# Optimization experiments

Measured on AMD Instinct MI355X. Metric: run time of the kernel, lower is better.

The kernel has to match this reference:

```python
import jax, jax.numpy as jnp
import numpy as np

N = 50000


def gcn_conv(x, W, b, src, dst, deg_inv_sqrt):
    # h = x @ W, then symmetric-normalized aggregation with self-loops
    h = x @ W  # [N, out]
    norm = deg_inv_sqrt[src] * deg_inv_sqrt[dst]  # [E]
    agg = jax.ops.segment_sum(h[src] * norm[:, None], dst, num_segments=N)
    # self-loop contribution: norm_ii = deg_inv_sqrt[i]^2
    agg = agg + h * (deg_inv_sqrt * deg_inv_sqrt)[:, None]
    return agg + b


def setup_inputs() -> dict:
    key = jax.random.key(0)
    ks = jax.random.split(key, 8)
    F_in, H, C = 128, 128, 64
    x = jax.random.normal(ks[0], (N, F_in), dtype=jnp.float32)
    edge_index = jax.random.randint(ks[1], (2, 800000), 0, N, dtype=jnp.int64)
    s = 1.0 / np.sqrt(F_in)
    W1 = jax.random.uniform(ks[2], (F_in, H), jnp.float32, -s, s)
    b1 = jnp.zeros((H,), jnp.float32)
    W2 = jax.random.uniform(ks[3], (H, H), jnp.float32, -s, s)
    b2 = jnp.zeros((H,), jnp.float32)
    W3 = jax.random.uniform(ks[4], (H, C), jnp.float32, -s, s)
    b3 = jnp.zeros((C,), jnp.float32)
    return {"x": x, "edge_index": edge_index, "W1": W1, "b1": b1,
            "W2": W2, "b2": b2, "W3": W3, "b3": b3}


def reference(x, edge_index, W1, b1, W2, b2, W3, b3):
    src, dst = edge_index[0], edge_index[1]
    # degree with self-loops (edge weight 1): deg[i] = in-degree + 1
    deg = jnp.zeros((N,), x.dtype).at[dst].add(1.0) + 1.0
    dinv = jax.lax.rsqrt(deg)
    h = gcn_conv(x, W1, b1, src, dst, dinv)
    h = jax.nn.relu(h)  # dropout p=0 / eval -> identity
    h = gcn_conv(h, W2, b2, src, dst, dinv)
    h = jax.nn.relu(h)
    h = gcn_conv(h, W3, b3, src, dst, dinv)
    return jax.nn.log_softmax(h, axis=-1)
```

## Files before the change

kernel.cpp:

```cpp
#include <hip/hip_runtime.h>
#include <math.h>

typedef short short8 __attribute__((ext_vector_type(8)));
typedef float floatx4 __attribute__((ext_vector_type(4)));

#define CHUNK_SHIFT 13
#define NCHUNK 8

__device__ __forceinline__ float4 ld4(const float* p) { return *reinterpret_cast<const float4*>(p); }
__device__ __forceinline__ void st4(float* p, float4 v) { *reinterpret_cast<float4*>(p) = v; }

__device__ __forceinline__ float bf2f(unsigned int u) { return __uint_as_float(u << 16); }
__device__ __forceinline__ unsigned int f2bf1(float f) {
    unsigned int x = __float_as_uint(f);
    return (x + 0x7fffu + ((x >> 16) & 1u)) >> 16;
}
__device__ __forceinline__ unsigned int f2bf2(float lo, float hi) {
    return f2bf1(lo) | (f2bf1(hi) << 16);
}
__device__ __forceinline__ void unpack8(uint4 v, float* f) {
    f[0] = bf2f(v.x & 0xffffu); f[1] = bf2f(v.x >> 16);
    f[2] = bf2f(v.y & 0xffffu); f[3] = bf2f(v.y >> 16);
    f[4] = bf2f(v.z & 0xffffu); f[5] = bf2f(v.z >> 16);
    f[6] = bf2f(v.w & 0xffffu); f[7] = bf2f(v.w >> 16);
}

__device__ __forceinline__ int sum8(const int* __restrict__ p) {
    uint4 a = *reinterpret_cast<const uint4*>(p);
    uint4 b = *reinterpret_cast<const uint4*>(p + 4);
    return (int)(a.x + a.y + a.z + a.w + b.x + b.y + b.z + b.w);
}

__global__ __launch_bounds__(256) void k_count_prep(const int* __restrict__ src, const int* __restrict__ dst,
                                                    int* __restrict__ deg2, int* __restrict__ rank, int E, int nbE,
                                                    const float* __restrict__ W1, const float* __restrict__ W2,
                                                    const float* __restrict__ W3, unsigned short* __restrict__ Wt1,
                                                    unsigned short* __restrict__ Wt2, unsigned short* __restrict__ Wt3) {
    if ((int)blockIdx.x < nbE) {
        int e = blockIdx.x * 256 + threadIdx.x;
        if (e < E) {
            int c = src[e] >> CHUNK_SHIFT;
            rank[e] = atomicAdd(&deg2[dst[e] * NCHUNK + c], 1);
        }
    } else {
        int t = (blockIdx.x - nbE) * 256 + threadIdx.x;
        if (t < 16384) {
            int k = t & 127, n = t >> 7;
            Wt1[n * 128 + k] = (unsigned short)f2bf1(W1[(size_t)k * 128 + n]);
        } else if (t < 32768) {
            int u = t - 16384;
            int k = u & 127, n = u >> 7;
            Wt2[n * 128 + k] = (unsigned short)f2bf1(W2[(size_t)k * 128 + n]);
        } else if (t < 40960) {
            int u = t - 32768;
            int k = u & 127, n = u >> 7;
            Wt3[n * 128 + k] = (unsigned short)f2bf1(W3[(size_t)k * 64 + n]);
        }
    }
}

__global__ __launch_bounds__(256) void k_dinv_reduce(const int* __restrict__ deg2, float* __restrict__ dinv,
                                                     int* __restrict__ bsum, int* __restrict__ hist,
                                                     int n, int nbN) {
    __shared__ int s[256];
    __shared__ int lh[64];
    int t = threadIdx.x;
    if ((int)blockIdx.x < nbN) {
        if (t < 64) lh[t] = 0;
        __syncthreads();
        int i = blockIdx.x * 256 + t;
        if (i < n) {
            int d = sum8(deg2 + (size_t)i * NCHUNK);
            dinv[i] = 1.0f / sqrtf((float)d + 1.0f);
            atomicAdd(&lh[min(d, 63)], 1);
        }
        __syncthreads();
        if (t < 64 && lh[t] != 0) atomicAdd(&hist[t], lh[t]);
        return;
    }
    int b = (int)blockIdx.x - nbN;
    int i = b * 256 + t;
    s[t] = (i < n) ? sum8(deg2 + (size_t)i * NCHUNK) : 0;
    __syncthreads();
    for (int off = 128; off > 0; off >>= 1) {
        if (t < off) s[t] += s[t + off];
        __syncthreads();
    }
    if (t == 0) bsum[b] = s[0];
}

__global__ __launch_bounds__(256) void k_scansmall_gemm1(const int* __restrict__ bsum, int* __restrict__ boff, int nb,
                                                         const int* __restrict__ hist, int* __restrict__ histcur,
                                                         const float* __restrict__ X, const unsigned short* __restrict__ Wt,
                                                         const float* __restrict__ dinv,
                                                         unsigned short* __restrict__ O, int nrows) {
    constexpr int LDR = 136;
    __shared__ __align__(16) unsigned char smem[(64 * LDR + 128 * LDR) * 2];

    const int tid = threadIdx.x;
    if (blockIdx.x == 0) {
        int* s = (int*)smem;
        int v = (tid < nb) ? bsum[tid] : 0;
        s[tid] = v;
        __syncthreads();
        for (int off = 1; off < 256; off <<= 1) {
            int x = (tid >= off) ? s[tid - off] : 0;
            __syncthreads();
            s[tid] += x;
            __syncthreads();
        }
        if (tid < nb) boff[tid] = s[tid] - v;
        return;
    }
    if (blockIdx.x == 1) {
        int* hsc = (int*)smem;
        if (tid < 64) hsc[tid] = hist[tid];
        __syncthreads();
        if (tid == 0) {
            int run = 0;
            for (int c = 0; c < 64; ++c) { int v = hsc[c]; hsc[c] = run; run += v; }
        }
        __syncthreads();
        if (tid < 64) histcur[tid] = hsc[tid];
        return;
    }

    unsigned short* sX = (unsigned short*)smem;
    unsigned short* sB = sX + 64 * LDR;
    const int row0 = ((int)blockIdx.x - 2) * 64;

#pragma unroll
    for (int i = 0; i < 4; ++i) {
        int idx = tid + i * 256;
        int r = idx >> 4, c8 = idx & 15;
        int grow = row0 + r;
        uint4 v = make_uint4(0, 0, 0, 0);
        if (grow < nrows) {
            float4 a = ld4(X + (size_t)grow * 128 + c8 * 8);
            float4 b = ld4(X + (size_t)grow * 128 + c8 * 8 + 4);
            v = make_uint4(f2bf2(a.x, a.y), f2bf2(a.z, a.w), f2bf2(b.x, b.y), f2bf2(b.z, b.w));
        }
        *reinterpret_cast<uint4*>(&sX[r * LDR + c8 * 8]) = v;
    }
#pragma unroll
    for (int i = 0; i < 8; ++i) {
        int idx = tid + i * 256;
        int nn = idx >> 4, c8 = idx & 15;
        *reinterpret_cast<uint4*>(&sB[nn * LDR + c8 * 8]) =
            *reinterpret_cast<const uint4*>(Wt + (size_t)nn * 128 + c8 * 8);
    }
    __syncthreads();

    const int lane = tid & 63;
    const int wave = tid >> 6;
    const int l15  = lane & 15;
    const int quad = lane >> 4;

    floatx4 acc[8];
#pragma unroll
    for (int j = 0; j < 8; ++j) acc[j] = (floatx4){0.f, 0.f, 0.f, 0.f};

    const unsigned short* xbase = &sX[(wave * 16 + l15) * LDR + quad * 8];
#pragma unroll
    for (int kk = 0; kk < 4; ++kk) {
        short8 xb = *reinterpret_cast<const short8*>(xbase + kk * 32);
#pragma unroll
        for (int j = 0; j < 8; ++j) {
            short8 wa = *reinterpret_cast<const short8*>(&sB[(j * 16 + l15) * LDR + quad * 8 + kk * 32]);
            acc[j] = __builtin_amdgcn_mfma_f32_16x16x32_bf16(wa, xb, acc[j], 0, 0, 0);
        }
    }

    int xrow = row0 + wave * 16 + l15;
    if (xrow < nrows) {
        float di = dinv[xrow];
#pragma unroll
        for (int j = 0; j < 8; ++j) {
            uint2 o = make_uint2(f2bf2(acc[j][0] * di, acc[j][1] * di), f2bf2(acc[j][2] * di, acc[j][3] * di));
            *reinterpret_cast<uint2*>(O + (size_t)xrow * 128 + j * 16 + quad * 4) = o;
        }
    }
}

__global__ __launch_bounds__(256) void k_scan_final(const int* __restrict__ deg2, const int* __restrict__ boff,
                                                    int* __restrict__ row_off, int* __restrict__ starts2,
                                                    int* __restrict__ histcur,
                                                    int* __restrict__ perm, int n, int nb) {
    __shared__ int s[256];
    __shared__ int lh[64];
    __shared__ int lbase[64];
    int t = threadIdx.x;
    if ((int)blockIdx.x < nb) {
        int i = blockIdx.x * 256 + t;
        uint4 d0 = make_uint4(0, 0, 0, 0), d1 = make_uint4(0, 0, 0, 0);
        int tot = 0;
        if (i < n) {
            d0 = *reinterpret_cast<const uint4*>(deg2 + (size_t)i * NCHUNK);
            d1 = *reinterpret_cast<const uint4*>(deg2 + (size_t)i * NCHUNK + 4);
            tot = (int)(d0.x + d0.y + d0.z + d0.w + d1.x + d1.y + d1.z + d1.w);
        }
        s[t] = tot;
        __syncthreads();
        for (int off = 1; off < 256; off <<= 1) {
            int x = (t >= off) ? s[t - off] : 0;
            __syncthreads();
            s[t] += x;
            __syncthreads();
        }
        int incl = s[t] + boff[blockIdx.x];
        if (i < n) {
            int r = incl - tot;
            row_off[i] = r;
            uint4 o0, o1;
            o0.x = r; r += d0.x;
            o0.y = r; r += d0.y;
            o0.z = r; r += d0.z;
            o0.w = r; r += d0.w;
            o1.x = r; r += d1.x;
            o1.y = r; r += d1.y;
            o1.z = r; r += d1.z;
            o1.w = r;
            *reinterpret_cast<uint4*>(starts2 + (size_t)i * NCHUNK) = o0;
            *reinterpret_cast<uint4*>(starts2 + (size_t)i * NCHUNK + 4) = o1;
            if (i == n - 1) row_off[n] = incl;
        }
        return;
    }
    int b = (int)blockIdx.x - nb;
    int i = b * 256 + t;
    if (t < 64) lh[t] = 0;
    __syncthreads();
    int c = 0, myr = 0;
    bool valid = (i < n);
    if (valid) {
        c = min(sum8(deg2 + (size_t)i * NCHUNK), 63);
        myr = atomicAdd(&lh[c], 1);
    }
    __syncthreads();
    if (t < 64 && lh[t] != 0) lbase[t] = atomicAdd(&histcur[t], lh[t]);
    __syncthreads();
    if (valid) perm[lbase[c] + myr] = i;
}

__global__ __launch_bounds__(256) void k_fill(const int* __restrict__ src, const int* __restrict__ dst,
                                              const int* __restrict__ rank, const int* __restrict__ starts2,
                                              int* __restrict__ csrc, int E) {
    int e = blockIdx.x * 256 + threadIdx.x;
    if (e < E) {
        int s = src[e];
        int c = s >> CHUNK_SHIFT;
        csrc[starts2[dst[e] * NCHUNK + c] + rank[e]] = s;
    }
}

template <int NC>
__global__ __launch_bounds__(256) void k_gemm_mfma(const unsigned short* __restrict__ X,
                                                   const unsigned short* __restrict__ Wt,
                                                   const float* __restrict__ dinv,
                                                   unsigned short* __restrict__ O, int nrows) {
    constexpr int LDR = 136;
    __shared__ unsigned short sX[64 * LDR];
    __shared__ unsigned short sB[NC * LDR];

    const int tid  = threadIdx.x;
    const int row0 = blockIdx.x * 64;

#pragma unroll
    for (int i = 0; i < 4; ++i) {
        int idx = tid + i * 256;
        int r = idx >> 4, c8 = idx & 15;
        int grow = row0 + r;
        uint4 v = make_uint4(0, 0, 0, 0);
        if (grow < nrows) v = *reinterpret_cast<const uint4*>(X + (size_t)grow * 128 + c8 * 8);
        *reinterpret_cast<uint4*>(&sX[r * LDR + c8 * 8]) = v;
    }
#pragma unroll
    for (int i = 0; i < NC / 16; ++i) {
        int idx = tid + i * 256;
        int n = idx >> 4, c8 = idx & 15;
        *reinterpret_cast<uint4*>(&sB[n * LDR + c8 * 8]) =
            *reinterpret_cast<const uint4*>(Wt + (size_t)n * 128 + c8 * 8);
    }
    __syncthreads();

    const int lane = tid & 63;
    const int wave = tid >> 6;
    const int l15  = lane & 15;
    const int quad = lane >> 4;

    floatx4 acc[NC / 16];
#pragma unroll
    for (int j = 0; j < NC / 16; ++j) acc[j] = (floatx4){0.f, 0.f, 0.f, 0.f};

    const unsigned short* xbase = &sX[(wave * 16 + l15) * LDR + quad * 8];
#pragma unroll
    for (int kk = 0; kk < 4; ++kk) {
        short8 xb = *reinterpret_cast<const short8*>(xbase + kk * 32);
#pragma unroll
        for (int j = 0; j < NC / 16; ++j) {
            short8 wa = *reinterpret_cast<const short8*>(&sB[(j * 16 + l15) * LDR + quad * 8 + kk * 32]);
            acc[j] = __builtin_amdgcn_mfma_f32_16x16x32_bf16(wa, xb, acc[j], 0, 0, 0);
        }
    }

    int xrow = row0 + wave * 16 + l15;
    if (xrow < nrows) {
        float di = dinv[xrow];
#pragma unroll
        for (int j = 0; j < NC / 16; ++j) {
            uint2 o = make_uint2(f2bf2(acc[j][0] * di, acc[j][1] * di), f2bf2(acc[j][2] * di, acc[j][3] * di));
            *reinterpret_cast<uint2*>(O + (size_t)xrow * NC + j * 16 + quad * 4) = o;
        }
    }
}

__global__ __launch_bounds__(256) void k_agg_relu(const unsigned short* __restrict__ H, const int* __restrict__ roff,
                                                  const int* __restrict__ csrc, const float* __restrict__ dinv,
                                                  const float* __restrict__ bias, const int* __restrict__ perm,
                                                  unsigned short* __restrict__ O, int n) {
    int t    = blockIdx.x * 256 + threadIdx.x;
    int g    = t >> 4;
    int f8   = (t & 15) * 8;
    if (g >= n) return;
    int node = perm[g];

    float a[8];
    {
        uint4 hv = *reinterpret_cast<const uint4*>(H + (size_t)node * 128 + f8);
        unpack8(hv, a);
    }

    int e  = roff[node];
    int e1 = roff[node + 1];
    for (; e + 3 < e1; e += 4) {
        int s[4];
        uint4 v[4];
#pragma unroll
        for (int u = 0; u < 4; ++u) s[u] = csrc[e + u];
#pragma unroll
        for (int u = 0; u < 4; ++u) v[u] = *reinterpret_cast<const uint4*>(H + (size_t)s[u] * 128 + f8);
#pragma unroll
        for (int u = 0; u < 4; ++u) {
            float g2[8];
            unpack8(v[u], g2);
#pragma unroll
            for (int i = 0; i < 8; ++i) a[i] += g2[i];
        }
    }
    for (; e < e1; ++e) {
        uint4 v0 = *reinterpret_cast<const uint4*>(H + (size_t)csrc[e] * 128 + f8);
        float g0[8];
        unpack8(v0, g0);
#pragma unroll
        for (int i = 0; i < 8; ++i) a[i] += g0[i];
    }

    float di = dinv[node];
    float4 b0 = ld4(bias + f8);
    float4 b1 = ld4(bias + f8 + 4);
    float bb[8] = {b0.x, b0.y, b0.z, b0.w, b1.x, b1.y, b1.z, b1.w};
#pragma unroll
    for (int i = 0; i < 8; ++i) a[i] = fmaxf(a[i] * di + bb[i], 0.0f);

    uint4 ov = make_uint4(f2bf2(a[0], a[1]), f2bf2(a[2], a[3]), f2bf2(a[4], a[5]), f2bf2(a[6], a[7]));
    *reinterpret_cast<uint4*>(O + (size_t)node * 128 + f8) = ov;
}

__global__ __launch_bounds__(256) void k_agg_softmax(const unsigned short* __restrict__ H, const int* __restrict__ roff,
                                                     const int* __restrict__ csrc, const float* __restrict__ dinv,
                                                     const float* __restrict__ bias, const int* __restrict__ perm,
                                                     float* __restrict__ O, int n) {
    int t    = blockIdx.x * 256 + threadIdx.x;
    int g    = t >> 3;
    int f8   = (t & 7) * 8;
    if (g >= n) return;
    int node = perm[g];

    float a[8];
    {
        uint4 hv = *reinterpret_cast<const uint4*>(H + (size_t)node * 64 + f8);
        unpack8(hv, a);
    }

    int e  = roff[node];
    int e1 = roff[node + 1];
    for (; e + 7 < e1; e += 8) {
        int s[8];
        uint4 v[8];
#pragma unroll
        for (int u = 0; u < 8; ++u) s[u] = csrc[e + u];
#pragma unroll
        for (int u = 0; u < 8; ++u) v[u] = *reinterpret_cast<const uint4*>(H + (size_t)s[u] * 64 + f8);
#pragma unroll
        for (int u = 0; u < 8; ++u) {
            float gg[8];
            unpack8(v[u], gg);
#pragma unroll
            for (int i = 0; i < 8; ++i) a[i] += gg[i];
        }
    }
    if (e + 3 < e1) {
        int s[4];
        uint4 v[4];
#pragma unroll
        for (int u = 0; u < 4; ++u) s[u] = csrc[e + u];
#pragma unroll
        for (int u = 0; u < 4; ++u) v[u] = *reinterpret_cast<const uint4*>(H + (size_t)s[u] * 64 + f8);
#pragma unroll
        for (int u = 0; u < 4; ++u) {
            float gg[8];
            unpack8(v[u], gg);
#pragma unroll
            for (int i = 0; i < 8; ++i) a[i] += gg[i];
        }
        e += 4;
    }
    for (; e < e1; ++e) {
        uint4 v0 = *reinterpret_cast<const uint4*>(H + (size_t)csrc[e] * 64 + f8);
        float g0[8];
        unpack8(v0, g0);
#pragma unroll
        for (int i = 0; i < 8; ++i) a[i] += g0[i];
    }

    float di = dinv[node];
    float4 b0 = ld4(bias + f8);
    float4 b1 = ld4(bias + f8 + 4);
    float bb[8] = {b0.x, b0.y, b0.z, b0.w, b1.x, b1.y, b1.z, b1.w};
    float v[8];
#pragma unroll
    for (int i = 0; i < 8; ++i) v[i] = a[i] * di + bb[i];

    float m = v[0];
#pragma unroll
    for (int i = 1; i < 8; ++i) m = fmaxf(m, v[i]);
    m = fmaxf(m, __shfl_xor(m, 1));
    m = fmaxf(m, __shfl_xor(m, 2));
    m = fmaxf(m, __shfl_xor(m, 4));

    float ssum = 0.0f;
#pragma unroll
    for (int i = 0; i < 8; ++i) ssum += expf(v[i] - m);
    ssum += __shfl_xor(ssum, 1);
    ssum += __shfl_xor(ssum, 2);
    ssum += __shfl_xor(ssum, 4);
    float ls = logf(ssum);

    float* op = O + (size_t)node * 64 + f8;
    st4(op, make_float4(v[0] - m - ls, v[1] - m - ls, v[2] - m - ls, v[3] - m - ls));
    st4(op + 4, make_float4(v[4] - m - ls, v[5] - m - ls, v[6] - m - ls, v[7] - m - ls));
}

extern "C" void kernel_launch(void* const* d_in, const int* in_sizes, int n_in,
                              void* d_out, int out_size, void* d_ws, size_t ws_size,
                              hipStream_t stream) {
    const float* x  = (const float*)d_in[0];
    const int*   ei = (const int*)d_in[1];
    const float* W1 = (const float*)d_in[2];
    const float* b1 = (const float*)d_in[3];
    const float* W2 = (const float*)d_in[4];
    const float* b2 = (const float*)d_in[5];
    const float* W3 = (const float*)d_in[6];
    const float* b3 = (const float*)d_in[7];
    float* out = (float*)d_out;

    const int N = in_sizes[0] / 128;
    const int E = in_sizes[1] / 2;
    const int* src = ei;
    const int* dst = ei + E;

    char* ws = (char*)d_ws;
    size_t off = 0;
    auto alloc = [&](size_t bytes) -> char* {
        char* p = ws + off;
        off = (off + bytes + 255) & ~(size_t)255;
        return p;
    };
    int nb  = (N + 255) / 256;
    int nbE = (E + 255) / 256;
    int blocks64 = (N + 63) / 64;

    int*   deg2    = (int*)alloc((size_t)N * NCHUNK * 4);
    int*   hist    = (int*)alloc(64 * 4);
    int*   histcur = (int*)alloc(64 * 4);
    int*   row_off = (int*)alloc(((size_t)N + 1) * 4);
    int*   starts2 = (int*)alloc((size_t)N * NCHUNK * 4);
    float* dinv    = (float*)alloc((size_t)N * 4);
    int*   bsum    = (int*)alloc((size_t)nb * 4);
    int*   boff    = (int*)alloc((size_t)nb * 4);
    int*   rank    = (int*)alloc((size_t)E * 4);
    int*   csrc    = (int*)alloc((size_t)E * 4);
    int*   perm    = (int*)alloc((size_t)N * 4);
    unsigned short* Wt1  = (unsigned short*)alloc(128 * 128 * 2);
    unsigned short* Wt2  = (unsigned short*)alloc(128 * 128 * 2);
    unsigned short* Wt3  = (unsigned short*)alloc(64 * 128 * 2);
    unsigned short* bufA = (unsigned short*)alloc((size_t)N * 128 * 2);
    unsigned short* bufB = (unsigned short*)alloc((size_t)N * 128 * 2);
    unsigned short* bufC = (unsigned short*)alloc((size_t)N * 64 * 2);
    (void)ws_size; (void)n_in; (void)out_size;

    size_t degPad = (((size_t)N * NCHUNK * 4 + 255) & ~(size_t)255);
    hipMemsetAsync(deg2, 0, degPad + 256, stream);
    k_count_prep<<<nbE + 160, 256, 0, stream>>>(src, dst, deg2, rank, E, nbE, W1, W2, W3, Wt1, Wt2, Wt3);
    k_dinv_reduce<<<nb + nb, 256, 0, stream>>>(deg2, dinv, bsum, hist, N, nb);
    k_scansmall_gemm1<<<2 + blocks64, 256, 0, stream>>>(bsum, boff, nb, hist, histcur, x, Wt1, dinv, bufA, N);
    k_scan_final<<<nb + nb, 256, 0, stream>>>(deg2, boff, row_off, starts2, histcur, perm, N, nb);
    k_fill<<<nbE, 256, 0, stream>>>(src, dst, rank, starts2, csrc, E);

    k_agg_relu<<<((size_t)N * 16 + 255) / 256, 256, 0, stream>>>(bufA, row_off, csrc, dinv, b1, perm, bufB, N);
    k_gemm_mfma<128><<<blocks64, 256, 0, stream>>>(bufB, Wt2, dinv, bufA, N);
    k_agg_relu<<<((size_t)N * 16 + 255) / 256, 256, 0, stream>>>(bufA, row_off, csrc, dinv, b2, perm, bufB, N);
    k_gemm_mfma<64><<<blocks64, 256, 0, stream>>>(bufB, Wt3, dinv, bufC, N);
    k_agg_softmax<<<((size_t)N * 8 + 255) / 256, 256, 0, stream>>>(bufC, row_off, csrc, dinv, b3, perm, out, N);
}
```

Measured before the change: 252.6 us.

## Fuse aggregation into following GEMM and drop degree-sorted node permutation

The separate aggregate+ReLU kernel and the MFMA GEMM kernel for layers 1 and 2 are merged into one k_agg_gemm kernel. Each block gathers neighbour rows for its 64 nodes, applies bias and ReLU, writes the bf16 result straight into shared memory and runs the MFMA from there, so the intermediate buffer never round-trips through global memory. The degree histogram and permutation sort (hist, histcur, perm) are removed entirely, and nodes are processed in natural order. The fused kernel uses only 782 blocks, and unbalanced degrees within a block cause warp divergence, so latency hiding in the gather may get worse.

```diff
diff --git a/kernel.cpp b/kernel.cpp
--- a/kernel.cpp
+++ b/kernel.cpp
@@ -60,22 +60,15 @@
 }
 
 __global__ __launch_bounds__(256) void k_dinv_reduce(const int* __restrict__ deg2, float* __restrict__ dinv,
-                                                     int* __restrict__ bsum, int* __restrict__ hist,
-                                                     int n, int nbN) {
+                                                     int* __restrict__ bsum, int n, int nbN) {
     __shared__ int s[256];
-    __shared__ int lh[64];
     int t = threadIdx.x;
     if ((int)blockIdx.x < nbN) {
-        if (t < 64) lh[t] = 0;
-        __syncthreads();
         int i = blockIdx.x * 256 + t;
         if (i < n) {
             int d = sum8(deg2 + (size_t)i * NCHUNK);
             dinv[i] = 1.0f / sqrtf((float)d + 1.0f);
-            atomicAdd(&lh[min(d, 63)], 1);
-        }
-        __syncthreads();
-        if (t < 64 && lh[t] != 0) atomicAdd(&hist[t], lh[t]);
+        }
         return;
     }
     int b = (int)blockIdx.x - nbN;
@@ -90,7 +83,6 @@
 }
 
 __global__ __launch_bounds__(256) void k_scansmall_gemm1(const int* __restrict__ bsum, int* __restrict__ boff, int nb,
-                                                         const int* __restrict__ hist, int* __restrict__ histcur,
                                                          const float* __restrict__ X, const unsigned short* __restrict__ Wt,
                                                          const float* __restrict__ dinv,
                                                          unsigned short* __restrict__ O, int nrows) {
@@ -112,22 +104,10 @@
         if (tid < nb) boff[tid] = s[tid] - v;
         return;
     }
-    if (blockIdx.x == 1) {
-        int* hsc = (int*)smem;
-        if (tid < 64) hsc[tid] = hist[tid];
-        __syncthreads();
-        if (tid == 0) {
-            int run = 0;
-            for (int c = 0; c < 64; ++c) { int v = hsc[c]; hsc[c] = run; run += v; }
-        }
-        __syncthreads();
-        if (tid < 64) histcur[tid] = hsc[tid];
-        return;
-    }
 
     unsigned short* sX = (unsigned short*)smem;
     unsigned short* sB = sX + 64 * LDR;
-    const int row0 = ((int)blockIdx.x - 2) * 64;
+    const int row0 = ((int)blockIdx.x - 1) * 64;
 
 #pragma unroll
     for (int i = 0; i < 4; ++i) {
@@ -184,62 +164,42 @@
 
 __global__ __launch_bounds__(256) void k_scan_final(const int* __restrict__ deg2, const int* __restrict__ boff,
                                                     int* __restrict__ row_off, int* __restrict__ starts2,
-                                                    int* __restrict__ histcur,
-                                                    int* __restrict__ perm, int n, int nb) {
+                                                    int n) {
     __shared__ int s[256];
-    __shared__ int lh[64];
-    __shared__ int lbase[64];
     int t = threadIdx.x;
-    if ((int)blockIdx.x < nb) {
-        int i = blockIdx.x * 256 + t;
-        uint4 d0 = make_uint4(0, 0, 0, 0), d1 = make_uint4(0, 0, 0, 0);
-        int tot = 0;
-        if (i < n) {
-            d0 = *reinterpret_cast<const uint4*>(deg2 + (size_t)i * NCHUNK);
-            d1 = *reinterpret_cast<const uint4*>(deg2 + (size_t)i * NCHUNK + 4);
-            tot = (int)(d0.x + d0.y + d0.z + d0.w + d1.x + d1.y + d1.z + d1.w);
-        }
-        s[t] = tot;
+    int i = blockIdx.x * 256 + t;
+    uint4 d0 = make_uint4(0, 0, 0, 0), d1 = make_uint4(0, 0, 0, 0);
+    int tot = 0;
+    if (i < n) {
+        d0 = *reinterpret_cast<const uint4*>(deg2 + (size_t)i * NCHUNK);
+        d1 = *reinterpret_cast<const uint4*>(deg2 + (size_t)i * NCHUNK + 4);
+        tot = (int)(d0.x + d0.y + d0.z + d0.w + d1.x + d1.y + d1.z + d1.w);
+    }
+    s[t] = tot;
+    __syncthreads();
+    for (int off = 1; off < 256; off <<= 1) {
+        int x = (t >= off) ? s[t - off] : 0;
         __syncthreads();
-        for (int off = 1; off < 256; off <<= 1) {
-            int x = (t >= off) ? s[t - off] : 0;
-            __syncthreads();
-            s[t] += x;
-            __syncthreads();
-        }
-        int incl = s[t] + boff[blockIdx.x];
-        if (i < n) {
-            int r = incl - tot;
-            row_off[i] = r;
-            uint4 o0, o1;
-            o0.x = r; r += d0.x;
-            o0.y = r; r += d0.y;
-            o0.z = r; r += d0.z;
-            o0.w = r; r += d0.w;
-            o1.x = r; r += d1.x;
-            o1.y = r; r += d1.y;
-            o1.z = r; r += d1.z;
-            o1.w = r;
-            *reinterpret_cast<uint4*>(starts2 + (size_t)i * NCHUNK) = o0;
-            *reinterpret_cast<uint4*>(starts2 + (size_t)i * NCHUNK + 4) = o1;
-            if (i == n - 1) row_off[n] = incl;
-        }
-        return;
-    }
-    int b = (int)blockIdx.x - nb;
-    int i = b * 256 + t;
-    if (t < 64) lh[t] = 0;
-    __syncthreads();
-    int c = 0, myr = 0;
-    bool valid = (i < n);
-    if (valid) {
-        c = min(sum8(deg2 + (size_t)i * NCHUNK), 63);
-        myr = atomicAdd(&lh[c], 1);
-    }
-    __syncthreads();
-    if (t < 64 && lh[t] != 0) lbase[t] = atomicAdd(&histcur[t], lh[t]);
-    __syncthreads();
-    if (valid) perm[lbase[c] + myr] = i;
+        s[t] += x;
+        __syncthreads();
+    }
+    int incl = s[t] + boff[blockIdx.x];
+    if (i < n) {
+        int r = incl - tot;
+        row_off[i] = r;
+        uint4 o0, o1;
+        o0.x = r; r += d0.x;
+        o0.y = r; r += d0.y;
+        o0.z = r; r += d0.z;
+        o0.w = r; r += d0.w;
+        o1.x = r; r += d1.x;
+        o1.y = r; r += d1.y;
+        o1.z = r; r += d1.z;
+        o1.w = r;
+        *reinterpret_cast<uint4*>(starts2 + (size_t)i * NCHUNK) = o0;
+        *reinterpret_cast<uint4*>(starts2 + (size_t)i * NCHUNK + 4) = o1;
+        if (i == n - 1) row_off[n] = incl;
+    }
 }
 
 __global__ __launch_bounds__(256) void k_fill(const int* __restrict__ src, const int* __restrict__ dst,
@@ -254,10 +214,13 @@
 }
 
 template <int NC>
-__global__ __launch_bounds__(256) void k_gemm_mfma(const unsigned short* __restrict__ X,
-                                                   const unsigned short* __restrict__ Wt,
-                                                   const float* __restrict__ dinv,
-                                                   unsigned short* __restrict__ O, int nrows) {
+__global__ __launch_bounds__(256) void k_agg_gemm(const unsigned short* __restrict__ H,
+                                                  const int* __restrict__ roff,
+                                                  const int* __restrict__ csrc,
+                                                  const float* __restrict__ dinv,
+                                                  const float* __restrict__ bias,
+                                                  const unsigned short* __restrict__ Wt,
+                                                  unsigned short* __restrict__ O, int n) {
     constexpr int LDR = 136;
     __shared__ unsigned short sX[64 * LDR];
     __shared__ unsigned short sB[NC * LDR];
@@ -266,20 +229,74 @@
     const int row0 = blockIdx.x * 64;
 
 #pragma unroll
-    for (int i = 0; i < 4; ++i) {
-        int idx = tid + i * 256;
-        int r = idx >> 4, c8 = idx & 15;
-        int grow = row0 + r;
-        uint4 v = make_uint4(0, 0, 0, 0);
-        if (grow < nrows) v = *reinterpret_cast<const uint4*>(X + (size_t)grow * 128 + c8 * 8);
-        *reinterpret_cast<uint4*>(&sX[r * LDR + c8 * 8]) = v;
-    }
-#pragma unroll
     for (int i = 0; i < NC / 16; ++i) {
         int idx = tid + i * 256;
-        int n = idx >> 4, c8 = idx & 15;
-        *reinterpret_cast<uint4*>(&sB[n * LDR + c8 * 8]) =
-            *reinterpret_cast<const uint4*>(Wt + (size_t)n * 128 + c8 * 8);
+        int nn = idx >> 4, c8 = idx & 15;
+        *reinterpret_cast<uint4*>(&sB[nn * LDR + c8 * 8]) =
+            *reinterpret_cast<const uint4*>(Wt + (size_t)nn * 128 + c8 * 8);
+    }
+
+    const int nl = tid >> 4;
+    const int f8 = (tid & 15) * 8;
+
+    float a[4][8];
+    int e[4], e1[4];
+#pragma unroll
+    for (int s = 0; s < 4; ++s) {
+        int node = row0 + s * 16 + nl;
+        if (node < n) {
+            uint4 hv = *reinterpret_cast<const uint4*>(H + (size_t)node * 128 + f8);
+            unpack8(hv, a[s]);
+            e[s]  = roff[node];
+            e1[s] = roff[node + 1];
+        } else {
+#pragma unroll
+            for (int i = 0; i < 8; ++i) a[s][i] = 0.0f;
+            e[s] = 0; e1[s] = 0;
+        }
+    }
+
+    int mb = 0;
+#pragma unroll
+    for (int s = 0; s < 4; ++s) mb = max(mb, (e1[s] - e[s] + 3) >> 2);
+
+    for (int b = 0; b < mb; ++b) {
+#pragma unroll
+        for (int s = 0; s < 4; ++s) {
+            if (e[s] >= e1[s]) continue;
+            int idx[4]; float mk[4];
+#pragma unroll
+            for (int u = 0; u < 4; ++u) {
+                bool ok = (e[s] + u) < e1[s];
+                idx[u] = ok ? csrc[e[s] + u] : 0;
+                mk[u]  = ok ? 1.0f : 0.0f;
+            }
+            uint4 v[4];
+#pragma unroll
+            for (int u = 0; u < 4; ++u) v[u] = *reinterpret_cast<const uint4*>(H + (size_t)idx[u] * 128 + f8);
+#pragma unroll
+            for (int u = 0; u < 4; ++u) {
+                float g[8];
+                unpack8(v[u], g);
+#pragma unroll
+                for (int i = 0; i < 8; ++i) a[s][i] = fmaf(mk[u], g[i], a[s][i]);
+            }
+            e[s] += 4;
+        }
+    }
+
+    float4 b0 = ld4(bias + f8);
+    float4 b1 = ld4(bias + f8 + 4);
+    float bb[8] = {b0.x, b0.y, b0.z, b0.w, b1.x, b1.y, b1.z, b1.w};
+#pragma unroll
+    for (int s = 0; s < 4; ++s) {
+        int node = row0 + s * 16 + nl;
+        float di = (node < n) ? dinv[node] : 0.0f;
+#pragma unroll
+        for (int i = 0; i < 8; ++i) a[s][i] = fmaxf(a[s][i] * di + bb[i], 0.0f);
+        uint4 ov = make_uint4(f2bf2(a[s][0], a[s][1]), f2bf2(a[s][2], a[s][3]),
+                              f2bf2(a[s][4], a[s][5]), f2bf2(a[s][6], a[s][7]));
+        *reinterpret_cast<uint4*>(&sX[(s * 16 + nl) * LDR + f8]) = ov;
     }
     __syncthreads();
 
@@ -304,7 +321,7 @@
     }
 
     int xrow = row0 + wave * 16 + l15;
-    if (xrow < nrows) {
+    if (xrow < n) {
         float di = dinv[xrow];
 #pragma unroll
         for (int j = 0; j < NC / 16; ++j) {
@@ -314,67 +331,13 @@
     }
 }
 
-__global__ __launch_bounds__(256) void k_agg_relu(const unsigned short* __restrict__ H, const int* __restrict__ roff,
-                                                  const int* __restrict__ csrc, const float* __restrict__ dinv,
-                                                  const float* __restrict__ bias, const int* __restrict__ perm,
-                                                  unsigned short* __restrict__ O, int n) {
-    int t    = blockIdx.x * 256 + threadIdx.x;
-    int g    = t >> 4;
-    int f8   = (t & 15) * 8;
-    if (g >= n) return;
-    int node = perm[g];
-
-    float a[8];
-    {
-        uint4 hv = *reinterpret_cast<const uint4*>(H + (size_t)node * 128 + f8);
-        unpack8(hv, a);
-    }
-
-    int e  = roff[node];
-    int e1 = roff[node + 1];
-    for (; e + 3 < e1; e += 4) {
-        int s[4];
-        uint4 v[4];
-#pragma unroll
-        for (int u = 0; u < 4; ++u) s[u] = csrc[e + u];
-#pragma unroll
-        for (int u = 0; u < 4; ++u) v[u] = *reinterpret_cast<const uint4*>(H + (size_t)s[u] * 128 + f8);
-#pragma unroll
-        for (int u = 0; u < 4; ++u) {
-            float g2[8];
-            unpack8(v[u], g2);
-#pragma unroll
-            for (int i = 0; i < 8; ++i) a[i] += g2[i];
-        }
-    }
-    for (; e < e1; ++e) {
-        uint4 v0 = *reinterpret_cast<const uint4*>(H + (size_t)csrc[e] * 128 + f8);
-        float g0[8];
-        unpack8(v0, g0);
-#pragma unroll
-        for (int i = 0; i < 8; ++i) a[i] += g0[i];
-    }
-
-    float di = dinv[node];
-    float4 b0 = ld4(bias + f8);
-    float4 b1 = ld4(bias + f8 + 4);
-    float bb[8] = {b0.x, b0.y, b0.z, b0.w, b1.x, b1.y, b1.z, b1.w};
-#pragma unroll
-    for (int i = 0; i < 8; ++i) a[i] = fmaxf(a[i] * di + bb[i], 0.0f);
-
-    uint4 ov = make_uint4(f2bf2(a[0], a[1]), f2bf2(a[2], a[3]), f2bf2(a[4], a[5]), f2bf2(a[6], a[7]));
-    *reinterpret_cast<uint4*>(O + (size_t)node * 128 + f8) = ov;
-}
-
 __global__ __launch_bounds__(256) void k_agg_softmax(const unsigned short* __restrict__ H, const int* __restrict__ roff,
                                                      const int* __restrict__ csrc, const float* __restrict__ dinv,
-                                                     const float* __restrict__ bias, const int* __restrict__ perm,
-                                                     float* __restrict__ O, int n) {
+                                                     const float* __restrict__ bias, float* __restrict__ O, int n) {
     int t    = blockIdx.x * 256 + threadIdx.x;
-    int g    = t >> 3;
+    int node = t >> 3;
     int f8   = (t & 7) * 8;
-    if (g >= n) return;
-    int node = perm[g];
+    if (node >= n) return;
 
     float a[8];
     {
@@ -481,8 +444,6 @@
     int blocks64 = (N + 63) / 64;
 
     int*   deg2    = (int*)alloc((size_t)N * NCHUNK * 4);
-    int*   hist    = (int*)alloc(64 * 4);
-    int*   histcur = (int*)alloc(64 * 4);
     int*   row_off = (int*)alloc(((size_t)N + 1) * 4);
     int*   starts2 = (int*)alloc((size_t)N * NCHUNK * 4);
     float* dinv    = (float*)alloc((size_t)N * 4);
@@ -490,7 +451,6 @@
     int*   boff    = (int*)alloc((size_t)nb * 4);
     int*   rank    = (int*)alloc((size_t)E * 4);
     int*   csrc    = (int*)alloc((size_t)E * 4);
-    int*   perm    = (int*)alloc((size_t)N * 4);
     unsigned short* Wt1  = (unsigned short*)alloc(128 * 128 * 2);
     unsigned short* Wt2  = (unsigned short*)alloc(128 * 128 * 2);
     unsigned short* Wt3  = (unsigned short*)alloc(64 * 128 * 2);
@@ -499,17 +459,14 @@
     unsigned short* bufC = (unsigned short*)alloc((size_t)N * 64 * 2);
     (void)ws_size; (void)n_in; (void)out_size;
 
-    size_t degPad = (((size_t)N * NCHUNK * 4 + 255) & ~(size_t)255);
-    hipMemsetAsync(deg2, 0, degPad + 256, stream);
+    hipMemsetAsync(deg2, 0, (size_t)N * NCHUNK * 4, stream);
     k_count_prep<<<nbE + 160, 256, 0, stream>>>(src, dst, deg2, rank, E, nbE, W1, W2, W3, Wt1, Wt2, Wt3);
-    k_dinv_reduce<<<nb + nb, 256, 0, stream>>>(deg2, dinv, bsum, hist, N, nb);
-    k_scansmall_gemm1<<<2 + blocks64, 256, 0, stream>>>(bsum, boff, nb, hist, histcur, x, Wt1, dinv, bufA, N);
-    k_scan_final<<<nb + nb, 256, 0, stream>>>(deg2, boff, row_off, starts2, histcur, perm, N, nb);
+    k_dinv_reduce<<<nb + nb, 256, 0, stream>>>(deg2, dinv, bsum, N, nb);
+    k_scansmall_gemm1<<<1 + blocks64, 256, 0, stream>>>(bsum, boff, nb, x, Wt1, dinv, bufA, N);
+    k_scan_final<<<nb, 256, 0, stream>>>(deg2, boff, row_off, starts2, N);
     k_fill<<<nbE, 256, 0, stream>>>(src, dst, rank, starts2, csrc, E);
 
-    k_agg_relu<<<((size_t)N * 16 + 255) / 256, 256, 0, stream>>>(bufA, row_off, csrc, dinv, b1, perm, bufB, N);
-    k_gemm_mfma<128><<<blocks64, 256, 0, stream>>>(bufB, Wt2, dinv, bufA, N);
-    k_agg_relu<<<((size_t)N * 16 + 255) / 256, 256, 0, stream>>>(bufA, row_off, csrc, dinv, b2, perm, bufB, N);
-    k_gemm_mfma<64><<<blocks64, 256, 0, stream>>>(bufB, Wt3, dinv, bufC, N);
-    k_agg_softmax<<<((size_t)N * 8 + 255) / 256, 256, 0, stream>>>(bufC, row_off, csrc, dinv, b3, perm, out, N);
-}
+    k_agg_gemm<128><<<blocks64, 256, 0, stream>>>(bufA, row_off, csrc, dinv, b1, Wt2, bufB, N);
+    k_agg_gemm<64><<<blocks64, 256, 0, stream>>>(bufB, row_off, csrc, dinv, b2, Wt3, bufC, N);
+    k_agg_softmax<<<((size_t)N * 8 + 255) / 256, 256, 0, stream>>>(bufC, row_off, csrc, dinv, b3, out, N);
+}
```

Result: slower. 271.8 us (+7.6%).

## Replace degree-sorted node permutation with split-edge two-group aggregation per node

Applied to the files above, without the earlier changes.

Removes the degree histogram, its scan and the permutation that ordered nodes by degree for load balance. Instead each node is processed by twice as many lanes, with the edge list split in half between two lane groups whose partial sums are combined by a cross-lane shuffle. This cuts several preprocessing steps and the indirect perm lookup, and doubles memory-level parallelism per node. In exchange, wavefronts can be imbalanced across differing degrees, and the second lane group idles during the epilogue.

```diff
diff --git a/kernel.cpp b/kernel.cpp
--- a/kernel.cpp
+++ b/kernel.cpp
@@ -60,22 +60,15 @@
 }
 
 __global__ __launch_bounds__(256) void k_dinv_reduce(const int* __restrict__ deg2, float* __restrict__ dinv,
-                                                     int* __restrict__ bsum, int* __restrict__ hist,
-                                                     int n, int nbN) {
+                                                     int* __restrict__ bsum, int n, int nbN) {
     __shared__ int s[256];
-    __shared__ int lh[64];
     int t = threadIdx.x;
     if ((int)blockIdx.x < nbN) {
-        if (t < 64) lh[t] = 0;
-        __syncthreads();
         int i = blockIdx.x * 256 + t;
         if (i < n) {
             int d = sum8(deg2 + (size_t)i * NCHUNK);
             dinv[i] = 1.0f / sqrtf((float)d + 1.0f);
-            atomicAdd(&lh[min(d, 63)], 1);
-        }
-        __syncthreads();
-        if (t < 64 && lh[t] != 0) atomicAdd(&hist[t], lh[t]);
+        }
         return;
     }
     int b = (int)blockIdx.x - nbN;
@@ -90,7 +83,6 @@
 }
 
 __global__ __launch_bounds__(256) void k_scansmall_gemm1(const int* __restrict__ bsum, int* __restrict__ boff, int nb,
-                                                         const int* __restrict__ hist, int* __restrict__ histcur,
                                                          const float* __restrict__ X, const unsigned short* __restrict__ Wt,
                                                          const float* __restrict__ dinv,
                                                          unsigned short* __restrict__ O, int nrows) {
@@ -112,22 +104,10 @@
         if (tid < nb) boff[tid] = s[tid] - v;
         return;
     }
-    if (blockIdx.x == 1) {
-        int* hsc = (int*)smem;
-        if (tid < 64) hsc[tid] = hist[tid];
-        __syncthreads();
-        if (tid == 0) {
-            int run = 0;
-            for (int c = 0; c < 64; ++c) { int v = hsc[c]; hsc[c] = run; run += v; }
-        }
-        __syncthreads();
-        if (tid < 64) histcur[tid] = hsc[tid];
-        return;
-    }
 
     unsigned short* sX = (unsigned short*)smem;
     unsigned short* sB = sX + 64 * LDR;
-    const int row0 = ((int)blockIdx.x - 2) * 64;
+    const int row0 = ((int)blockIdx.x - 1) * 64;
 
 #pragma unroll
     for (int i = 0; i < 4; ++i) {
@@ -184,62 +164,42 @@
 
 __global__ __launch_bounds__(256) void k_scan_final(const int* __restrict__ deg2, const int* __restrict__ boff,
                                                     int* __restrict__ row_off, int* __restrict__ starts2,
-                                                    int* __restrict__ histcur,
-                                                    int* __restrict__ perm, int n, int nb) {
+                                                    int n) {
     __shared__ int s[256];
-    __shared__ int lh[64];
-    __shared__ int lbase[64];
     int t = threadIdx.x;
-    if ((int)blockIdx.x < nb) {
-        int i = blockIdx.x * 256 + t;
-        uint4 d0 = make_uint4(0, 0, 0, 0), d1 = make_uint4(0, 0, 0, 0);
-        int tot = 0;
-        if (i < n) {
-            d0 = *reinterpret_cast<const uint4*>(deg2 + (size_t)i * NCHUNK);
-            d1 = *reinterpret_cast<const uint4*>(deg2 + (size_t)i * NCHUNK + 4);
-            tot = (int)(d0.x + d0.y + d0.z + d0.w + d1.x + d1.y + d1.z + d1.w);
-        }
-        s[t] = tot;
+    int i = blockIdx.x * 256 + t;
+    uint4 d0 = make_uint4(0, 0, 0, 0), d1 = make_uint4(0, 0, 0, 0);
+    int tot = 0;
+    if (i < n) {
+        d0 = *reinterpret_cast<const uint4*>(deg2 + (size_t)i * NCHUNK);
+        d1 = *reinterpret_cast<const uint4*>(deg2 + (size_t)i * NCHUNK + 4);
+        tot = (int)(d0.x + d0.y + d0.z + d0.w + d1.x + d1.y + d1.z + d1.w);
+    }
+    s[t] = tot;
+    __syncthreads();
+    for (int off = 1; off < 256; off <<= 1) {
+        int x = (t >= off) ? s[t - off] : 0;
         __syncthreads();
-        for (int off = 1; off < 256; off <<= 1) {
-            int x = (t >= off) ? s[t - off] : 0;
-            __syncthreads();
-            s[t] += x;
-            __syncthreads();
-        }
-        int incl = s[t] + boff[blockIdx.x];
-        if (i < n) {
-            int r = incl - tot;
-            row_off[i] = r;
-            uint4 o0, o1;
-            o0.x = r; r += d0.x;
-            o0.y = r; r += d0.y;
-            o0.z = r; r += d0.z;
-            o0.w = r; r += d0.w;
-            o1.x = r; r += d1.x;
-            o1.y = r; r += d1.y;
-            o1.z = r; r += d1.z;
-            o1.w = r;
-            *reinterpret_cast<uint4*>(starts2 + (size_t)i * NCHUNK) = o0;
-            *reinterpret_cast<uint4*>(starts2 + (size_t)i * NCHUNK + 4) = o1;
-            if (i == n - 1) row_off[n] = incl;
-        }
-        return;
-    }
-    int b = (int)blockIdx.x - nb;
-    int i = b * 256 + t;
-    if (t < 64) lh[t] = 0;
-    __syncthreads();
-    int c = 0, myr = 0;
-    bool valid = (i < n);
-    if (valid) {
-        c = min(sum8(deg2 + (size_t)i * NCHUNK), 63);
-        myr = atomicAdd(&lh[c], 1);
-    }
-    __syncthreads();
-    if (t < 64 && lh[t] != 0) lbase[t] = atomicAdd(&histcur[t], lh[t]);
-    __syncthreads();
-    if (valid) perm[lbase[c] + myr] = i;
+        s[t] += x;
+        __syncthreads();
+    }
+    int incl = s[t] + boff[blockIdx.x];
+    if (i < n) {
+        int r = incl - tot;
+        row_off[i] = r;
+        uint4 o0, o1;
+        o0.x = r; r += d0.x;
+        o0.y = r; r += d0.y;
+        o0.z = r; r += d0.z;
+        o0.w = r; r += d0.w;
+        o1.x = r; r += d1.x;
+        o1.y = r; r += d1.y;
+        o1.z = r; r += d1.z;
+        o1.w = r;
+        *reinterpret_cast<uint4*>(starts2 + (size_t)i * NCHUNK) = o0;
+        *reinterpret_cast<uint4*>(starts2 + (size_t)i * NCHUNK + 4) = o1;
+        if (i == n - 1) row_off[n] = incl;
+    }
 }
 
 __global__ __launch_bounds__(256) void k_fill(const int* __restrict__ src, const int* __restrict__ dst,
@@ -316,23 +276,30 @@
 
 __global__ __launch_bounds__(256) void k_agg_relu(const unsigned short* __restrict__ H, const int* __restrict__ roff,
                                                   const int* __restrict__ csrc, const float* __restrict__ dinv,
-                                                  const float* __restrict__ bias, const int* __restrict__ perm,
-                                                  unsigned short* __restrict__ O, int n) {
-    int t    = blockIdx.x * 256 + threadIdx.x;
-    int g    = t >> 4;
-    int f8   = (t & 15) * 8;
-    if (g >= n) return;
-    int node = perm[g];
+                                                  const float* __restrict__ bias, unsigned short* __restrict__ O, int n) {
+    int t      = blockIdx.x * 256 + threadIdx.x;
+    int node   = t >> 5;
+    int lane32 = t & 31;
+    int half   = lane32 >> 4;
+    int f8     = (lane32 & 15) * 8;
+    if (node >= n) return;
 
     float a[8];
-    {
+    if (half == 0) {
         uint4 hv = *reinterpret_cast<const uint4*>(H + (size_t)node * 128 + f8);
         unpack8(hv, a);
-    }
-
-    int e  = roff[node];
+    } else {
+#pragma unroll
+        for (int i = 0; i < 8; ++i) a[i] = 0.0f;
+    }
+
+    int e0 = roff[node];
     int e1 = roff[node + 1];
-    for (; e + 3 < e1; e += 4) {
+    int mid = e0 + ((e1 - e0) >> 1);
+    int e  = half ? mid : e0;
+    int ee = half ? e1 : mid;
+
+    for (; e + 3 < ee; e += 4) {
         int s[4];
         uint4 v[4];
 #pragma unroll
@@ -347,7 +314,7 @@
             for (int i = 0; i < 8; ++i) a[i] += g2[i];
         }
     }
-    for (; e < e1; ++e) {
+    for (; e < ee; ++e) {
         uint4 v0 = *reinterpret_cast<const uint4*>(H + (size_t)csrc[e] * 128 + f8);
         float g0[8];
         unpack8(v0, g0);
@@ -355,51 +322,48 @@
         for (int i = 0; i < 8; ++i) a[i] += g0[i];
     }
 
-    float di = dinv[node];
-    float4 b0 = ld4(bias + f8);
-    float4 b1 = ld4(bias + f8 + 4);
-    float bb[8] = {b0.x, b0.y, b0.z, b0.w, b1.x, b1.y, b1.z, b1.w};
-#pragma unroll
-    for (int i = 0; i < 8; ++i) a[i] = fmaxf(a[i] * di + bb[i], 0.0f);
-
-    uint4 ov = make_uint4(f2bf2(a[0], a[1]), f2bf2(a[2], a[3]), f2bf2(a[4], a[5]), f2bf2(a[6], a[7]));
-    *reinterpret_cast<uint4*>(O + (size_t)node * 128 + f8) = ov;
+#pragma unroll
+    for (int i = 0; i < 8; ++i) a[i] += __shfl_xor(a[i], 16);
+
+    if (half == 0) {
+        float di = dinv[node];
+        float4 b0 = ld4(bias + f8);
+        float4 b1 = ld4(bias + f8 + 4);
+        float bb[8] = {b0.x, b0.y, b0.z, b0.w, b1.x, b1.y, b1.z, b1.w};
+#pragma unroll
+        for (int i = 0; i < 8; ++i) a[i] = fmaxf(a[i] * di + bb[i], 0.0f);
+
+        uint4 ov = make_uint4(f2bf2(a[0], a[1]), f2bf2(a[2], a[3]), f2bf2(a[4], a[5]), f2bf2(a[6], a[7]));
+        *reinterpret_cast<uint4*>(O + (size_t)node * 128 + f8) = ov;
+    }
 }
 
 __global__ __launch_bounds__(256) void k_agg_softmax(const unsigned short* __restrict__ H, const int* __restrict__ roff,
                                                      const int* __restrict__ csrc, const float* __restrict__ dinv,
-                                                     const float* __restrict__ bias, const int* __restrict__ perm,
-                                                     float* __restrict__ O, int n) {
-    int t    = blockIdx.x * 256 + threadIdx.x;
-    int g    = t >> 3;
-    int f8   = (t & 7) * 8;
-    if (g >= n) return;
-    int node = perm[g];
+                                                     const float* __restrict__ bias, float* __restrict__ O, int n) {
+    int t      = blockIdx.x * 256 + threadIdx.x;
+    int node   = t >> 4;
+    int lane16 = t & 15;
+    int half   = lane16 >> 3;
+    int f8     = (lane16 & 7) * 8;
+    if (node >= n) return;
 
     float a[8];
-    {
+    if (half == 0) {
         uint4 hv = *reinterpret_cast<const uint4*>(H + (size_t)node * 64 + f8);
         unpack8(hv, a);
-    }
-
-    int e  = roff[node];
+    } else {
+#pragma unroll
+        for (int i = 0; i < 8; ++i) a[i] = 0.0f;
+    }
+
+    int e0 = roff[node];
     int e1 = roff[node + 1];
-    for (; e + 7 < e1; e += 8) {
-        int s[8];
-        uint4 v[8];
-#pragma unroll
-        for (int u = 0; u < 8; ++u) s[u] = csrc[e + u];
-#pragma unroll
-        for (int u = 0; u < 8; ++u) v[u] = *reinterpret_cast<const uint4*>(H + (size_t)s[u] * 64 + f8);
-#pragma unroll
-        for (int u = 0; u < 8; ++u) {
-            float gg[8];
-            unpack8(v[u], gg);
-#pragma unroll
-            for (int i = 0; i < 8; ++i) a[i] += gg[i];
-        }
-    }
-    if (e + 3 < e1) {
+    int mid = e0 + ((e1 - e0) >> 1);
+    int e  = half ? mid : e0;
+    int ee = half ? e1 : mid;
+
+    for (; e + 3 < ee; e += 4) {
         int s[4];
         uint4 v[4];
 #pragma unroll
@@ -413,9 +377,8 @@
 #pragma unroll
             for (int i = 0; i < 8; ++i) a[i] += gg[i];
         }
-        e += 4;
-    }
-    for (; e < e1; ++e) {
+    }
+    for (; e < ee; ++e) {
         uint4 v0 = *reinterpret_cast<const uint4*>(H + (size_t)csrc[e] * 64 + f8);
         float g0[8];
         unpack8(v0, g0);
@@ -423,32 +386,37 @@
         for (int i = 0; i < 8; ++i) a[i] += g0[i];
     }
 
-    float di = dinv[node];
-    float4 b0 = ld4(bias + f8);
-    float4 b1 = ld4(bias + f8 + 4);
-    float bb[8] = {b0.x, b0.y, b0.z, b0.w, b1.x, b1.y, b1.z, b1.w};
-    float v[8];
-#pragma unroll
-    for (int i = 0; i < 8; ++i) v[i] = a[i] * di + bb[i];
-
-    float m = v[0];
-#pragma unroll
-    for (int i = 1; i < 8; ++i) m = fmaxf(m, v[i]);
-    m = fmaxf(m, __shfl_xor(m, 1));
-    m = fmaxf(m, __shfl_xor(m, 2));
-    m = fmaxf(m, __shfl_xor(m, 4));
-
-    float ssum = 0.0f;
-#pragma unroll
-    for (int i = 0; i < 8; ++i) ssum += expf(v[i] - m);
-    ssum += __shfl_xor(ssum, 1);
-    ssum += __shfl_xor(ssum, 2);
-    ssum += __shfl_xor(ssum, 4);
-    float ls = logf(ssum);
-
-    float* op = O + (size_t)node * 64 + f8;
-    st4(op, make_float4(v[0] - m - ls, v[1] - m - ls, v[2] - m - ls, v[3] - m - ls));
-    st4(op + 4, make_float4(v[4] - m - ls, v[5] - m - ls, v[6] - m - ls, v[7] - m - ls));
+#pragma unroll
+    for (int i = 0; i < 8; ++i) a[i] += __shfl_xor(a[i], 8);
+
+    if (half == 0) {
+        float di = dinv[node];
+        float4 b0 = ld4(bias + f8);
+        float4 b1 = ld4(bias + f8 + 4);
+        float bb[8] = {b0.x, b0.y, b0.z, b0.w, b1.x, b1.y, b1.z, b1.w};
+        float v[8];
+#pragma unroll
+        for (int i = 0; i < 8; ++i) v[i] = a[i] * di + bb[i];
+
+        float m = v[0];
+#pragma unroll
+        for (int i = 1; i < 8; ++i) m = fmaxf(m, v[i]);
+        m = fmaxf(m, __shfl_xor(m, 1));
+        m = fmaxf(m, __shfl_xor(m, 2));
+        m = fmaxf(m, __shfl_xor(m, 4));
+
+        float ssum = 0.0f;
+#pragma unroll
+        for (int i = 0; i < 8; ++i) ssum += expf(v[i] - m);
+        ssum += __shfl_xor(ssum, 1);
+        ssum += __shfl_xor(ssum, 2);
+        ssum += __shfl_xor(ssum, 4);
+        float ls = logf(ssum);
+
+        float* op = O + (size_t)node * 64 + f8;
+        st4(op, make_float4(v[0] - m - ls, v[1] - m - ls, v[2] - m - ls, v[3] - m - ls));
+        st4(op + 4, make_float4(v[4] - m - ls, v[5] - m - ls, v[6] - m - ls, v[7] - m - ls));
+    }
 }
 
 extern "C" void kernel_launch(void* const* d_in, const int* in_sizes, int n_in,
@@ -481,8 +449,6 @@
     int blocks64 = (N + 63) / 64;
 
     int*   deg2    = (int*)alloc((size_t)N * NCHUNK * 4);
-    int*   hist    = (int*)alloc(64 * 4);
-    int*   histcur = (int*)alloc(64 * 4);
     int*   row_off = (int*)alloc(((size_t)N + 1) * 4);
     int*   starts2 = (int*)alloc((size_t)N * NCHUNK * 4);
     float* dinv    = (float*)alloc((size_t)N * 4);
@@ -490,7 +456,6 @@
     int*   boff    = (int*)alloc((size_t)nb * 4);
     int*   rank    = (int*)alloc((size_t)E * 4);
     int*   csrc    = (int*)alloc((size_t)E * 4);
-    int*   perm    = (int*)alloc((size_t)N * 4);
     unsigned short* Wt1  = (unsigned short*)alloc(128 * 128 * 2);
     unsigned short* Wt2  = (unsigned short*)alloc(128 * 128 * 2);
     unsigned short* Wt3  = (unsigned short*)alloc(64 * 128 * 2);
@@ -499,17 +464,16 @@
     unsigned short* bufC = (unsigned short*)alloc((size_t)N * 64 * 2);
     (void)ws_size; (void)n_in; (void)out_size;
 
-    size_t degPad = (((size_t)N * NCHUNK * 4 + 255) & ~(size_t)255);
-    hipMemsetAsync(deg2, 0, degPad + 256, stream);
+    hipMemsetAsync(deg2, 0, (size_t)N * NCHUNK * 4, stream);
     k_count_prep<<<nbE + 160, 256, 0, stream>>>(src, dst, deg2, rank, E, nbE, W1, W2, W3, Wt1, Wt2, Wt3);
-    k_dinv_reduce<<<nb + nb, 256, 0, stream>>>(deg2, dinv, bsum, hist, N, nb);
-    k_scansmall_gemm1<<<2 + blocks64, 256, 0, stream>>>(bsum, boff, nb, hist, histcur, x, Wt1, dinv, bufA, N);
-    k_scan_final<<<nb + nb, 256, 0, stream>>>(deg2, boff, row_off, starts2, histcur, perm, N, nb);
+    k_dinv_reduce<<<nb + nb, 256, 0, stream>>>(deg2, dinv, bsum, N, nb);
+    k_scansmall_gemm1<<<1 + blocks64, 256, 0, stream>>>(bsum, boff, nb, x, Wt1, dinv, bufA, N);
+    k_scan_final<<<nb, 256, 0, stream>>>(deg2, boff, row_off, starts2, N);
     k_fill<<<nbE, 256, 0, stream>>>(src, dst, rank, starts2, csrc, E);
 
-    k_agg_relu<<<((size_t)N * 16 + 255) / 256, 256, 0, stream>>>(bufA, row_off, csrc, dinv, b1, perm, bufB, N);
+    k_agg_relu<<<((size_t)N * 32 + 255) / 256, 256, 0, stream>>>(bufA, row_off, csrc, dinv, b1, bufB, N);
     k_gemm_mfma<128><<<blocks64, 256, 0, stream>>>(bufB, Wt2, dinv, bufA, N);
-    k_agg_relu<<<((size_t)N * 16 + 255) / 256, 256, 0, stream>>>(bufA, row_off, csrc, dinv, b2, perm, bufB, N);
+    k_agg_relu<<<((size_t)N * 32 + 255) / 256, 256, 0, stream>>>(bufA, row_off, csrc, dinv, b2, bufB, N);
     k_gemm_mfma<64><<<blocks64, 256, 0, stream>>>(bufB, Wt3, dinv, bufC, N);
-    k_agg_softmax<<<((size_t)N * 8 + 255) / 256, 256, 0, stream>>>(bufC, row_off, csrc, dinv, b3, perm, out, N);
-}
+    k_agg_softmax<<<((size_t)N * 16 + 255) / 256, 256, 0, stream>>>(bufC, row_off, csrc, dinv, b3, out, N);
+}
```

Result: no change. 252.1 us (median of 2 runs) (-0.2%).
